# Optimization experiments

Measured on AMD Instinct MI355X. Metric: run time of the kernel, lower is better.

The kernel has to match this reference:

```python
import jax, jax.numpy as jnp
import numpy as np

K = 4  # Chebyshev order (layer._k)

def setup_inputs() -> dict:
    key = jax.random.key(0)
    k1, k2, k3, k4 = jax.random.split(key, 4)
    N, din, dout = 4096, 128, 128
    a = jax.random.normal(k1, (N, din), dtype=jnp.float32)            # layer input (only len used)
    r = jax.random.uniform(k2, (N, dout), dtype=jnp.float32)          # upstream relevance (positive)
    # sparse-ish binary directed adjacency, no self loops (avg degree ~16)
    adj = (jax.random.uniform(k3, (N, N)) < (16.0 / N)).astype(jnp.float32)
    adj = adj * (1.0 - jnp.eye(N, dtype=jnp.float32))
    W = jax.random.normal(k4, (dout, K * din), dtype=jnp.float32) * 0.05  # ChebConv linear weight [out, K*in]
    return {"a": a, "r": r, "adj": adj, "W": W}

def _forward(a, r, adj, W):
    N = a.shape[0]
    dW = W.shape[1] // K
    # Wk[k] = W[:, k*dW:(k+1)*dW].T  -> [K, dimY(in), dimJ(out)]; rho = abs
    rhoW = jnp.abs(jnp.stack([W[:, k * dW:(k + 1) * dW].T for k in range(K)]))
    # Laplacian: L = I - D^{-1/2} A D^{-1/2}, degrees clamped at 1 (in-degrees = column sums)
    dinv = jnp.clip(adj.sum(axis=0), 1.0, None) ** -0.5
    D = dinv[:, None] * adj * dinv[None, :]
    L = jnp.eye(N, dtype=adj.dtype) - D
    # Chebyshev polynomials T_0=I, T_1=L, T_k = 2 L T_{k-1} - T_{k-2}  -> [K, N, N]
    Ts = [jnp.eye(N, dtype=L.dtype), L]
    for _ in range(2, K):
        Ts.append(2.0 * (L @ Ts[-1]) - Ts[-2])
    Ak = jnp.stack(Ts[:K])
    # U[i,j,x,y] = sum_k Ak[k,i,x] * rhoW[k,y,j]; never materialized.
    # denom[i,j] = U.sum(dim=(2,3)) = sum_k (sum_x Ak[k,i,x]) * (sum_y rhoW[k,y,j])
    denom = jnp.einsum('ki,kj->ij', Ak.sum(axis=2), rhoW.sum(axis=1))
    c = r / denom
    # out[x,y] = einsum('ijxy,ij->xy', U, c) = sum_k Ak[k].T @ c @ rhoW[k].T
    return jnp.einsum('kix,kyj,ij->xy', Ak, rhoW, c)

def reference(a, r, adj, W):
    return _forward(a, r, adj, W)
```

## Files before the change

### kernel.cpp

```cpp
#include <hip/hip_runtime.h>
#include <cstdint>
#include <cstddef>

#define N_NODES 4096
#define FEAT 128
#define KCH 4
#define NNZ_CAP (1 << 18)
#define TB2 256
#define TB3 256
#define T2CAP 2048
#define RSTRIDE 96

__device__ __forceinline__ int panel_of(int p) {
    return p < 3456 ? (p / 384) : (p < 3776 ? 9 : 10);
}

__global__ __launch_bounds__(256) void k_adj(const float* __restrict__ adj,
                                             int* __restrict__ deg,
                                             int* __restrict__ rdeg,
                                             int* __restrict__ rcolF) {
    int row = (blockIdx.x * 256 + threadIdx.x) >> 6;
    int lane = threadIdx.x & 63;
    const float4* rowp = (const float4*)(adj + (size_t)row * N_NODES);
    int base = 0;
    for (int it = 0; it < 16; ++it) {
        float4 q = rowp[it * 64 + lane];
        int nib = (q.x != 0.0f) | ((q.y != 0.0f) << 1)
                | ((q.z != 0.0f) << 2) | ((q.w != 0.0f) << 3);
        int cnt = __popc(nib);
        int sc = cnt;
        for (int off = 1; off < 64; off <<= 1) {
            int n = __shfl_up(sc, off);
            if (lane >= off) sc += n;
        }
        int myoff = base + sc - cnt;
        int x0 = it * 256 + 4 * lane;
        #pragma unroll
        for (int c = 0; c < 4; ++c) {
            if (nib & (1 << c)) {
                if (myoff < RSTRIDE) rcolF[row * RSTRIDE + myoff] = x0 + c;
                atomicAdd(&deg[x0 + c], 1);
                ++myoff;
            }
        }
        base += __shfl(sc, 63);
    }
    if (lane == 0) rdeg[row] = (base > RSTRIDE) ? RSTRIDE : base;
}

__global__ __launch_bounds__(1024) void k_scan(const int* __restrict__ deg,
                                               float* __restrict__ dinv,
                                               int* __restrict__ colptr,
                                               int* __restrict__ colcur) {
    __shared__ int wsum[16];
    __shared__ int wbase[16];
    int t = threadIdx.x;
    int lane = t & 63, wv = t >> 6;
    int v[4]; int s = 0;
    for (int c = 0; c < 4; ++c) {
        int idx = t * 4 + c;
        int di = deg[idx];
        v[c] = di;
        s += di;
        float dc = fmaxf((float)di, 1.0f);
        dinv[idx] = (float)(1.0 / sqrt((double)dc));
    }
    int sc = s;
    for (int off = 1; off < 64; off <<= 1) {
        int n = __shfl_up(sc, off);
        if (lane >= off) sc += n;
    }
    if (lane == 63) wsum[wv] = sc;
    __syncthreads();
    if (t == 0) {
        int b = 0;
        for (int q2 = 0; q2 < 16; ++q2) { wbase[q2] = b; b += wsum[q2]; }
    }
    __syncthreads();
    int base = wbase[wv] + sc - s;
    for (int c = 0; c < 4; ++c) {
        int idx = t * 4 + c;
        colptr[idx] = base; colcur[idx] = base;
        base += v[c];
    }
    if (t == 1023) colptr[N_NODES] = base;
}

__global__ __launch_bounds__(256) void k_vals(const float* __restrict__ dinv,
                                              const int* __restrict__ rdeg,
                                              const int* __restrict__ rcolF,
                                              float* __restrict__ rlvalF,
                                              int* __restrict__ colcur,
                                              int* __restrict__ col_i,
                                              float* __restrict__ val,
                                              const float* __restrict__ W,
                                              float* __restrict__ sW) {
    if (blockIdx.x >= N_NODES / 4) {
        int tid = (blockIdx.x - N_NODES / 4) * 256 + threadIdx.x;
        int k = tid >> 7, j = tid & 127;
        float s = 0.f;
        for (int y = 0; y < FEAT; ++y)
            s += fabsf(W[(size_t)j * (KCH * FEAT) + k * FEAT + y]);
        sW[k * FEAT + j] = s;
        return;
    }
    int row = (blockIdx.x * 256 + threadIdx.x) >> 6;
    int lane = threadIdx.x & 63;
    int n = rdeg[row];
    float di = dinv[row];
    for (int e = lane; e < n; e += 64) {
        int x = rcolF[row * RSTRIDE + e];
        float dv = di * dinv[x];
        rlvalF[row * RSTRIDE + e] = -dv;
        int ec = atomicAdd(&colcur[x], 1);
        if (ec < NNZ_CAP) { col_i[ec] = row; val[ec] = dv; }
    }
}

__device__ __forceinline__ float np_pairwise_4096(const float* __restrict__ row,
                                                  float* r256, float* leaf,
                                                  float* bc, int t) {
    if (t < 256) {
        int L = t >> 3, j = t & 7;
        const float* p = row + L * 128 + j;
        float a = p[0];
        #pragma unroll
        for (int q = 1; q < 16; ++q) a += p[8 * q];
        r256[t] = a;
    }
    __syncthreads();
    if (t < 32) {
        const float* rr = r256 + t * 8;
        leaf[t] = ((rr[0] + rr[1]) + (rr[2] + rr[3])) + ((rr[4] + rr[5]) + (rr[6] + rr[7]));
    }
    __syncthreads();
    if (t == 0) {
        float v[32];
        #pragma unroll
        for (int q = 0; q < 32; ++q) v[q] = leaf[q];
        #pragma unroll
        for (int w = 16; w >= 1; w >>= 1)
            #pragma unroll
            for (int q = 0; q < 16; ++q)
                if (q < w) v[q] = v[2 * q] + v[2 * q + 1];
        bc[0] = v[0];
    }
    __syncthreads();
    float res = bc[0];
    __syncthreads();
    return res;
}

__global__ __launch_bounds__(TB2) void k_t2(const int* __restrict__ rdeg,
                                            const int* __restrict__ rcolF,
                                            const float* __restrict__ rlvalF,
                                            unsigned short* __restrict__ t2c,
                                            float* __restrict__ t2v,
                                            int* __restrict__ t2cnt,
                                            float* __restrict__ sA) {
    __shared__ float gp[N_NODES];
    __shared__ int   pcol[64];
    __shared__ float pLip[64];
    __shared__ int   pnn[64];
    __shared__ int   ssplit;
    __shared__ float r256[256], leaf[32], bc[1];
    __shared__ int   wtot[4], wbase[4];
    int t = threadIdx.x;
    int i = blockIdx.x;
    int rp = i * RSTRIDE;
    int ol = rdeg[i];
    int cnt = ol + 1;
    if (cnt > 64) cnt = 64;
    if (t == 0) ssplit = 0;
    __syncthreads();
    if (t < ol && rcolF[rp + t] < i) atomicAdd(&ssplit, 1);
    __syncthreads();
    int split = ssplit;
    if (t < cnt) {
        int col; float lip;
        if (t < split)       { col = rcolF[rp + t];     lip = rlvalF[rp + t]; }
        else if (t == split) { col = i;                 lip = 1.0f; }
        else                 { col = rcolF[rp + t - 1]; lip = rlvalF[rp + t - 1]; }
        pcol[t] = col; pLip[t] = lip; pnn[t] = rdeg[col];
    }
    float4* gp4 = (float4*)gp;
    const float4 z4 = make_float4(0.f, 0.f, 0.f, 0.f);
    #pragma unroll
    for (int u2 = 0; u2 < 4; ++u2) gp4[t + u2 * TB2] = z4;
    __syncthreads();
    for (int e = t; e < ol; e += TB2) gp[rcolF[rp + e]] = rlvalF[rp + e];
    if (t == 0) gp[i] = 1.0f;
    __syncthreads();
    float s1 = np_pairwise_4096(gp, r256, leaf, bc, t);
    for (int e = t; e < ol; e += TB2) gp[rcolF[rp + e]] = 0.0f;
    if (t == 0) gp[i] = 0.0f;
    __syncthreads();
    float tot[16];
    #pragma unroll
    for (int u = 0; u < 16; ++u) tot[u] = 0.0f;
    int q = 0;
    while (q < cnt) {
        {
            float lv = pLip[q];
            int p = pcol[q];
            int nn = pnn[q];
            int b = p * RSTRIDE;
            for (int e = t; e < nn; e += TB2)
                gp[rcolF[b + e]] = fmaf(lv, rlvalF[b + e], gp[rcolF[b + e]]);
            if (t == 0) gp[p] = fmaf(lv, 1.0f, gp[p]);
            __syncthreads();
        }
        ++q;
        if (q == cnt || panel_of(pcol[q]) != panel_of(pcol[q - 1])) {
            #pragma unroll
            for (int u2 = 0; u2 < 4; ++u2) {
                int idx = t + u2 * TB2;
                float4 b = gp4[idx];
                tot[4 * u2 + 0] = tot[4 * u2 + 0] + b.x;
                tot[4 * u2 + 1] = tot[4 * u2 + 1] + b.y;
                tot[4 * u2 + 2] = tot[4 * u2 + 2] + b.z;
                tot[4 * u2 + 3] = tot[4 * u2 + 3] + b.w;
                gp4[idx] = z4;
            }
            __syncthreads();
        }
    }
    #pragma unroll
    for (int u2 = 0; u2 < 4; ++u2) {
        int xb = 4 * t + 1024 * u2;
        float4 v;
        v.x = 2.0f * tot[4 * u2 + 0] - (xb + 0 == i ? 1.0f : 0.0f);
        v.y = 2.0f * tot[4 * u2 + 1] - (xb + 1 == i ? 1.0f : 0.0f);
        v.z = 2.0f * tot[4 * u2 + 2] - (xb + 2 == i ? 1.0f : 0.0f);
        v.w = 2.0f * tot[4 * u2 + 3] - (xb + 3 == i ? 1.0f : 0.0f);
        gp4[t + u2 * TB2] = v;
    }
    __syncthreads();
    float s2 = np_pairwise_4096(gp, r256, leaf, bc, t);
    float ev[16];
    #pragma unroll
    for (int u2 = 0; u2 < 4; ++u2) {
        float4 e4 = gp4[4 * t + u2];
        ev[4 * u2 + 0] = e4.x; ev[4 * u2 + 1] = e4.y;
        ev[4 * u2 + 2] = e4.z; ev[4 * u2 + 3] = e4.w;
    }
    int cl = 0;
    #pragma unroll
    for (int u = 0; u < 16; ++u) cl += (ev[u] != 0.0f);
    int lane = t & 63, wv = t >> 6;
    int sc = cl;
    for (int off = 1; off < 64; off <<= 1) {
        int n = __shfl_up(sc, off);
        if (lane >= off) sc += n;
    }
    if (lane == 63) wtot[wv] = sc;
    __syncthreads();
    if (t == 0) {
        int b = 0;
        for (int wq = 0; wq < 4; ++wq) { wbase[wq] = b; b += wtot[wq]; }
        t2cnt[i] = (b > T2CAP) ? T2CAP : b;
    }
    __syncthreads();
    int pos = wbase[wv] + sc - cl;
    unsigned short* dstc = t2c + (size_t)i * T2CAP;
    float* dstv = t2v + (size_t)i * T2CAP;
    #pragma unroll
    for (int u = 0; u < 16; ++u) {
        if (ev[u] != 0.0f) {
            if (pos < T2CAP) { dstc[pos] = (unsigned short)(t * 16 + u); dstv[pos] = ev[u]; }
            ++pos;
        }
    }
    if (t == 0) {
        sA[0 * N_NODES + i] = 1.0f;
        sA[1 * N_NODES + i] = s1;
        sA[2 * N_NODES + i] = s2;
    }
}

__global__ __launch_bounds__(TB3) void k_t3(const int* __restrict__ rdeg,
                                            const int* __restrict__ rcolF,
                                            const float* __restrict__ rlvalF,
                                            const unsigned short* __restrict__ t2c,
                                            const float* __restrict__ t2v,
                                            const int* __restrict__ t2cnt,
                                            float* __restrict__ sA) {
    __shared__ float gp[N_NODES];
    __shared__ int   pcol[64];
    __shared__ float pLip[64];
    __shared__ int   pnn[64];
    __shared__ int   ssplit;
    __shared__ float r256[256], leaf[32], bc[1];
    int t = threadIdx.x;
    int i = blockIdx.x;
    int rp = i * RSTRIDE;
    int ol = rdeg[i];
    int cnt = ol + 1;
    if (cnt > 64) cnt = 64;
    if (t == 0) ssplit = 0;
    __syncthreads();
    if (t < ol && rcolF[rp + t] < i) atomicAdd(&ssplit, 1);
    __syncthreads();
    int split = ssplit;
    if (t < cnt) {
        int col; float lip;
        if (t < split)       { col = rcolF[rp + t];     lip = rlvalF[rp + t]; }
        else if (t == split) { col = i;                  lip = 1.0f; }
        else                 { col = rcolF[rp + t - 1];  lip = rlvalF[rp + t - 1]; }
        pcol[t] = col; pLip[t] = lip; pnn[t] = t2cnt[col];
    }
    float4* gp4 = (float4*)gp;
    const float4 z4 = make_float4(0.f, 0.f, 0.f, 0.f);
    #pragma unroll
    for (int u2 = 0; u2 < 4; ++u2) gp4[t + u2 * TB3] = z4;
    __syncthreads();
    float tot[16];
    #pragma unroll
    for (int u = 0; u < 16; ++u) tot[u] = 0.0f;
    int q = 0;
    while (q < cnt) {
        {
            float lv = pLip[q];
            int nn = pnn[q];
            const unsigned short* spc = t2c + (size_t)pcol[q] * T2CAP;
            const float* spv = t2v + (size_t)pcol[q] * T2CAP;
            for (int e = t; e < nn; e += TB3) {
                int x = spc[e];
                gp[x] = fmaf(lv, spv[e], gp[x]);
            }
            __syncthreads();
        }
        ++q;
        if (q == cnt || panel_of(pcol[q]) != panel_of(pcol[q - 1])) {
            #pragma unroll
            for (int u2 = 0; u2 < 4; ++u2) {
                int idx = t + u2 * TB3;
                float4 b = gp4[idx];
                tot[4 * u2 + 0] = tot[4 * u2 + 0] + b.x;
                tot[4 * u2 + 1] = tot[4 * u2 + 1] + b.y;
                tot[4 * u2 + 2] = tot[4 * u2 + 2] + b.z;
                tot[4 * u2 + 3] = tot[4 * u2 + 3] + b.w;
                gp4[idx] = z4;
            }
            __syncthreads();
        }
    }
    #pragma unroll
    for (int u2 = 0; u2 < 4; ++u2) {
        float4 v;
        v.x = 2.0f * tot[4 * u2 + 0];
        v.y = 2.0f * tot[4 * u2 + 1];
        v.z = 2.0f * tot[4 * u2 + 2];
        v.w = 2.0f * tot[4 * u2 + 3];
        gp4[t + u2 * TB3] = v;
    }
    __syncthreads();
    for (int e = t; e < ol; e += TB3) { int x = rcolF[rp + e]; gp[x] = gp[x] - rlvalF[rp + e]; }
    if (t == 0) gp[i] = gp[i] - 1.0f;
    __syncthreads();
    float s3 = np_pairwise_4096(gp, r256, leaf, bc, t);
    if (t == 0) sA[3 * N_NODES + i] = s3;
}

__global__ __launch_bounds__(256) void k_cm(const float* __restrict__ r,
                                            const float* __restrict__ sA,
                                            const float* __restrict__ sW,
                                            const float* __restrict__ W,
                                            float* __restrict__ M) {
#pragma clang fp contract(off)
    __shared__ float cl[16][FEAT];
    int k = blockIdx.y;
    int ib = blockIdx.x * 16;
    int tx = threadIdx.x;
    int y = tx & 127, half = tx >> 7;
    for (int m = tx; m < 16 * FEAT; m += 256) {
        int i = ib + (m >> 7), j = m & 127;
        float denom = 0.0f;
        #pragma unroll
        for (int k2 = 0; k2 < KCH; ++k2) {
            float p = sA[k2 * N_NODES + i] * sW[k2 * FEAT + j];
            denom = denom + p;
        }
        cl[m >> 7][m & 127] = r[(size_t)i * FEAT + j] / denom;
    }
    __syncthreads();
    float acc[8];
    #pragma unroll
    for (int u = 0; u < 8; ++u) acc[u] = 0.0f;
    for (int j = 0; j < FEAT; ++j) {
        float a = fabsf(W[(size_t)j * (KCH * FEAT) + k * FEAT + y]);
        #pragma unroll
        for (int u = 0; u < 8; ++u) acc[u] += a * cl[half * 8 + u][j];
    }
    #pragma unroll
    for (int u = 0; u < 8; ++u)
        M[(size_t)k * N_NODES * FEAT + (size_t)(ib + half * 8 + u) * FEAT + y] = acc[u];
}

__global__ void k_h1(const int* __restrict__ colptr, const int* __restrict__ col_i,
                     const float* __restrict__ val, const float* __restrict__ M,
                     float* __restrict__ B2) {
    int x = blockIdx.x * 2 + (threadIdx.x >> 7);
    int y = threadIdx.x & 127;
    const float* M2 = M + (size_t)2 * N_NODES * FEAT;
    const float* M3 = M + (size_t)3 * N_NODES * FEAT;
    int e0 = colptr[x], e1 = colptr[x + 1];
    if (e1 > NNZ_CAP) e1 = NNZ_CAP;
    float g = 0.0f;
    for (int e = e0; e < e1; ++e)
        g += val[e] * M3[(size_t)col_i[e] * FEAT + y];
    size_t o = (size_t)x * FEAT + y;
    B2[o] = 2.0f * M2[o] + 4.0f * (M3[o] - g);
}

__global__ void k_h2(const int* __restrict__ colptr, const int* __restrict__ col_i,
                     const float* __restrict__ val, const float* __restrict__ M,
                     const float* __restrict__ B2, float* __restrict__ B3) {
    int x = blockIdx.x * 2 + (threadIdx.x >> 7);
    int y = threadIdx.x & 127;
    const float* M1 = M + (size_t)N_NODES * FEAT;
    const float* M3 = M + (size_t)3 * N_NODES * FEAT;
    int e0 = colptr[x], e1 = colptr[x + 1];
    if (e1 > NNZ_CAP) e1 = NNZ_CAP;
    float g = 0.0f;
    for (int e = e0; e < e1; ++e)
        g += val[e] * B2[(size_t)col_i[e] * FEAT + y];
    size_t o = (size_t)x * FEAT + y;
    B3[o] = (M1[o] - 3.0f * M3[o]) + (B2[o] - g);
}

__global__ void k_h3(const int* __restrict__ colptr, const int* __restrict__ col_i,
                     const float* __restrict__ val, const float* __restrict__ M,
                     const float* __restrict__ B3, float* __restrict__ out) {
    int x = blockIdx.x * 2 + (threadIdx.x >> 7);
    int y = threadIdx.x & 127;
    const float* M0 = M;
    const float* M2 = M + (size_t)2 * N_NODES * FEAT;
    int e0 = colptr[x], e1 = colptr[x + 1];
    if (e1 > NNZ_CAP) e1 = NNZ_CAP;
    float g = 0.0f;
    for (int e = e0; e < e1; ++e)
        g += val[e] * B3[(size_t)col_i[e] * FEAT + y];
    size_t o = (size_t)x * FEAT + y;
    out[o] = (M0[o] - M2[o]) + (B3[o] - g);
}

extern "C" void kernel_launch(void* const* d_in, const int* in_sizes, int n_in,
                              void* d_out, int out_size, void* d_ws, size_t ws_size,
                              hipStream_t stream) {
    const float* r   = (const float*)d_in[1];
    const float* adj = (const float*)d_in[2];
    const float* W   = (const float*)d_in[3];
    float* out = (float*)d_out;

    char* w = (char*)d_ws;
    auto take = [&](size_t bytes) {
        char* p = w;
        w += (bytes + 255) & ~(size_t)255;
        return p;
    };
    int*   deg    = (int*)take((size_t)N_NODES * 4);
    int*   rdeg   = (int*)take((size_t)N_NODES * 4);
    float* dinv   = (float*)take((size_t)N_NODES * 4);
    int*   colcur = (int*)take((size_t)N_NODES * 4);
    int*   colptr = (int*)take((size_t)(N_NODES + 1) * 4);
    int*   col_i  = (int*)take((size_t)NNZ_CAP * 4);
    float* val    = (float*)take((size_t)NNZ_CAP * 4);
    int*   rcolF  = (int*)take((size_t)N_NODES * RSTRIDE * 4);
    float* rlvalF = (float*)take((size_t)N_NODES * RSTRIDE * 4);
    float* sW     = (float*)take((size_t)KCH * FEAT * 4);
    float* sA     = (float*)take((size_t)KCH * N_NODES * 4);
    float* M      = (float*)take((size_t)KCH * N_NODES * FEAT * 4);
    float* B2     = (float*)take((size_t)N_NODES * FEAT * 4);
    float* B3     = (float*)take((size_t)N_NODES * FEAT * 4);
    int*   t2cnt  = (int*)take((size_t)N_NODES * 4);
    unsigned short* t2c = (unsigned short*)take((size_t)N_NODES * T2CAP * 2);
    float* t2v    = (float*)take((size_t)N_NODES * T2CAP * 4);

    hipMemsetAsync(deg, 0, (size_t)N_NODES * 4, stream);
    k_adj<<<N_NODES / 4, 256, 0, stream>>>(adj, deg, rdeg, rcolF);
    k_scan<<<1, 1024, 0, stream>>>(deg, dinv, colptr, colcur);
    k_vals<<<N_NODES / 4 + 2, 256, 0, stream>>>(dinv, rdeg, rcolF, rlvalF,
                                                colcur, col_i, val, W, sW);
    k_t2<<<N_NODES, TB2, 0, stream>>>(rdeg, rcolF, rlvalF, t2c, t2v, t2cnt, sA);
    k_t3<<<N_NODES, TB3, 0, stream>>>(rdeg, rcolF, rlvalF, t2c, t2v, t2cnt, sA);
    k_cm<<<dim3(N_NODES / 16, KCH), 256, 0, stream>>>(r, sA, sW, W, M);
    k_h1<<<N_NODES / 2, 256, 0, stream>>>(colptr, col_i, val, M, B2);
    k_h2<<<N_NODES / 2, 256, 0, stream>>>(colptr, col_i, val, M, B2, B3);
    k_h3<<<N_NODES / 2, 256, 0, stream>>>(colptr, col_i, val, M, B3, out);
}
```

Measured before the change: 306.6 us.

## Split T2/T3 row expansion into two column-half blocks with separate leaf reduction

```diff
diff --git a/kernel.cpp b/kernel.cpp
--- a/kernel.cpp
+++ b/kernel.cpp
@@ -6,9 +6,9 @@
 #define FEAT 128
 #define KCH 4
 #define NNZ_CAP (1 << 18)
-#define TB2 256
-#define TB3 256
-#define T2CAP 2048
+#define TBH 128
+#define HALF 2048
+#define T2HC 1024
 #define RSTRIDE 96
 
 __device__ __forceinline__ int panel_of(int p) {
@@ -117,56 +117,40 @@
     }
 }
 
-__device__ __forceinline__ float np_pairwise_4096(const float* __restrict__ row,
-                                                  float* r256, float* leaf,
-                                                  float* bc, int t) {
-    if (t < 256) {
-        int L = t >> 3, j = t & 7;
-        const float* p = row + L * 128 + j;
-        float a = p[0];
-        #pragma unroll
-        for (int q = 1; q < 16; ++q) a += p[8 * q];
-        r256[t] = a;
-    }
-    __syncthreads();
-    if (t < 32) {
-        const float* rr = r256 + t * 8;
-        leaf[t] = ((rr[0] + rr[1]) + (rr[2] + rr[3])) + ((rr[4] + rr[5]) + (rr[6] + rr[7]));
-    }
-    __syncthreads();
-    if (t == 0) {
-        float v[32];
-        #pragma unroll
-        for (int q = 0; q < 32; ++q) v[q] = leaf[q];
-        #pragma unroll
-        for (int w = 16; w >= 1; w >>= 1)
-            #pragma unroll
-            for (int q = 0; q < 16; ++q)
-                if (q < w) v[q] = v[2 * q] + v[2 * q + 1];
-        bc[0] = v[0];
-    }
-    __syncthreads();
-    float res = bc[0];
-    __syncthreads();
-    return res;
-}
-
-__global__ __launch_bounds__(TB2) void k_t2(const int* __restrict__ rdeg,
+__device__ __forceinline__ void np_leaves_half(const float* __restrict__ half,
+                                               float* r256h, float* lf, int t) {
+    const float* p = half + (t >> 3) * 128 + (t & 7);
+    float a = p[0];
+    #pragma unroll
+    for (int q = 1; q < 16; ++q) a += p[8 * q];
+    r256h[t] = a;
+    __syncthreads();
+    if (t < 16) {
+        const float* rr = r256h + t * 8;
+        lf[t] = ((rr[0] + rr[1]) + (rr[2] + rr[3])) + ((rr[4] + rr[5]) + (rr[6] + rr[7]));
+    }
+    __syncthreads();
+}
+
+__global__ __launch_bounds__(TBH) void k_t2(const int* __restrict__ rdeg,
                                             const int* __restrict__ rcolF,
                                             const float* __restrict__ rlvalF,
                                             unsigned short* __restrict__ t2c,
                                             float* __restrict__ t2v,
-                                            int* __restrict__ t2cnt,
-                                            float* __restrict__ sA) {
-    __shared__ float gp[N_NODES];
+                                            int* __restrict__ t2cnt2,
+                                            float* __restrict__ L1f,
+                                            float* __restrict__ L2f) {
+    __shared__ float gp[HALF];
     __shared__ int   pcol[64];
     __shared__ float pLip[64];
     __shared__ int   pnn[64];
     __shared__ int   ssplit;
-    __shared__ float r256[256], leaf[32], bc[1];
-    __shared__ int   wtot[4], wbase[4];
+    __shared__ float r256h[TBH], lf[16];
+    __shared__ int   wtot[2], wbase2[2];
     int t = threadIdx.x;
-    int i = blockIdx.x;
+    int bid = blockIdx.x;
+    int i = bid >> 1, h = bid & 1;
+    int base = h << 11;
     int rp = i * RSTRIDE;
     int ol = rdeg[i];
     int cnt = ol + 1;
@@ -186,14 +170,22 @@
     float4* gp4 = (float4*)gp;
     const float4 z4 = make_float4(0.f, 0.f, 0.f, 0.f);
     #pragma unroll
-    for (int u2 = 0; u2 < 4; ++u2) gp4[t + u2 * TB2] = z4;
-    __syncthreads();
-    for (int e = t; e < ol; e += TB2) gp[rcolF[rp + e]] = rlvalF[rp + e];
-    if (t == 0) gp[i] = 1.0f;
-    __syncthreads();
-    float s1 = np_pairwise_4096(gp, r256, leaf, bc, t);
-    for (int e = t; e < ol; e += TB2) gp[rcolF[rp + e]] = 0.0f;
-    if (t == 0) gp[i] = 0.0f;
+    for (int u2 = 0; u2 < 4; ++u2) gp4[t + u2 * TBH] = z4;
+    __syncthreads();
+    for (int e = t; e < ol; e += TBH) {
+        int x = rcolF[rp + e];
+        if ((x >> 11) == h) gp[x - base] = rlvalF[rp + e];
+    }
+    if (t == 0 && (i >> 11) == h) gp[i - base] = 1.0f;
+    __syncthreads();
+    np_leaves_half(gp, r256h, lf, t);
+    if (t < 16) L1f[(size_t)i * 32 + h * 16 + t] = lf[t];
+    __syncthreads();
+    for (int e = t; e < ol; e += TBH) {
+        int x = rcolF[rp + e];
+        if ((x >> 11) == h) gp[x - base] = 0.0f;
+    }
+    if (t == 0 && (i >> 11) == h) gp[i - base] = 0.0f;
     __syncthreads();
     float tot[16];
     #pragma unroll
@@ -205,21 +197,23 @@
             int p = pcol[q];
             int nn = pnn[q];
             int b = p * RSTRIDE;
-            for (int e = t; e < nn; e += TB2)
-                gp[rcolF[b + e]] = fmaf(lv, rlvalF[b + e], gp[rcolF[b + e]]);
-            if (t == 0) gp[p] = fmaf(lv, 1.0f, gp[p]);
+            for (int e = t; e < nn; e += TBH) {
+                int x = rcolF[b + e];
+                if ((x >> 11) == h) gp[x - base] = fmaf(lv, rlvalF[b + e], gp[x - base]);
+            }
+            if (t == 0 && (p >> 11) == h) gp[p - base] = fmaf(lv, 1.0f, gp[p - base]);
             __syncthreads();
         }
         ++q;
         if (q == cnt || panel_of(pcol[q]) != panel_of(pcol[q - 1])) {
             #pragma unroll
             for (int u2 = 0; u2 < 4; ++u2) {
-                int idx = t + u2 * TB2;
-                float4 b = gp4[idx];
-                tot[4 * u2 + 0] = tot[4 * u2 + 0] + b.x;
-                tot[4 * u2 + 1] = tot[4 * u2 + 1] + b.y;
-                tot[4 * u2 + 2] = tot[4 * u2 + 2] + b.z;
-                tot[4 * u2 + 3] = tot[4 * u2 + 3] + b.w;
+                int idx = t + u2 * TBH;
+                float4 b4 = gp4[idx];
+                tot[4 * u2 + 0] = tot[4 * u2 + 0] + b4.x;
+                tot[4 * u2 + 1] = tot[4 * u2 + 1] + b4.y;
+                tot[4 * u2 + 2] = tot[4 * u2 + 2] + b4.z;
+                tot[4 * u2 + 3] = tot[4 * u2 + 3] + b4.w;
                 gp4[idx] = z4;
             }
             __syncthreads();
@@ -227,16 +221,17 @@
     }
     #pragma unroll
     for (int u2 = 0; u2 < 4; ++u2) {
-        int xb = 4 * t + 1024 * u2;
+        int xg = base + 4 * t + 512 * u2;
         float4 v;
-        v.x = 2.0f * tot[4 * u2 + 0] - (xb + 0 == i ? 1.0f : 0.0f);
-        v.y = 2.0f * tot[4 * u2 + 1] - (xb + 1 == i ? 1.0f : 0.0f);
-        v.z = 2.0f * tot[4 * u2 + 2] - (xb + 2 == i ? 1.0f : 0.0f);
-        v.w = 2.0f * tot[4 * u2 + 3] - (xb + 3 == i ? 1.0f : 0.0f);
-        gp4[t + u2 * TB2] = v;
-    }
-    __syncthreads();
-    float s2 = np_pairwise_4096(gp, r256, leaf, bc, t);
+        v.x = 2.0f * tot[4 * u2 + 0] - (xg + 0 == i ? 1.0f : 0.0f);
+        v.y = 2.0f * tot[4 * u2 + 1] - (xg + 1 == i ? 1.0f : 0.0f);
+        v.z = 2.0f * tot[4 * u2 + 2] - (xg + 2 == i ? 1.0f : 0.0f);
+        v.w = 2.0f * tot[4 * u2 + 3] - (xg + 3 == i ? 1.0f : 0.0f);
+        gp4[t + u2 * TBH] = v;
+    }
+    __syncthreads();
+    np_leaves_half(gp, r256h, lf, t);
+    if (t < 16) L2f[(size_t)i * 32 + h * 16 + t] = lf[t];
     float ev[16];
     #pragma unroll
     for (int u2 = 0; u2 < 4; ++u2) {
@@ -256,43 +251,44 @@
     if (lane == 63) wtot[wv] = sc;
     __syncthreads();
     if (t == 0) {
-        int b = 0;
-        for (int wq = 0; wq < 4; ++wq) { wbase[wq] = b; b += wtot[wq]; }
-        t2cnt[i] = (b > T2CAP) ? T2CAP : b;
-    }
-    __syncthreads();
-    int pos = wbase[wv] + sc - cl;
-    unsigned short* dstc = t2c + (size_t)i * T2CAP;
-    float* dstv = t2v + (size_t)i * T2CAP;
+        int b = wtot[0];
+        wbase2[0] = 0; wbase2[1] = b;
+        b += wtot[1];
+        t2cnt2[bid] = (b > T2HC) ? T2HC : b;
+    }
+    __syncthreads();
+    int pos = wbase2[wv] + sc - cl;
+    unsigned short* dstc = t2c + (size_t)bid * T2HC;
+    float* dstv = t2v + (size_t)bid * T2HC;
     #pragma unroll
     for (int u = 0; u < 16; ++u) {
         if (ev[u] != 0.0f) {
-            if (pos < T2CAP) { dstc[pos] = (unsigned short)(t * 16 + u); dstv[pos] = ev[u]; }
+            if (pos < T2HC) {
+                dstc[pos] = (unsigned short)(base + t * 16 + u);
+                dstv[pos] = ev[u];
+            }
             ++pos;
         }
     }
-    if (t == 0) {
-        sA[0 * N_NODES + i] = 1.0f;
-        sA[1 * N_NODES + i] = s1;
-        sA[2 * N_NODES + i] = s2;
-    }
-}
-
-__global__ __launch_bounds__(TB3) void k_t3(const int* __restrict__ rdeg,
+}
+
+__global__ __launch_bounds__(TBH) void k_t3(const int* __restrict__ rdeg,
                                             const int* __restrict__ rcolF,
                                             const float* __restrict__ rlvalF,
                                             const unsigned short* __restrict__ t2c,
                                             const float* __restrict__ t2v,
-                                            const int* __restrict__ t2cnt,
-                                            float* __restrict__ sA) {
-    __shared__ float gp[N_NODES];
+                                            const int* __restrict__ t2cnt2,
+                                            float* __restrict__ L3f) {
+    __shared__ float gp[HALF];
     __shared__ int   pcol[64];
     __shared__ float pLip[64];
     __shared__ int   pnn[64];
     __shared__ int   ssplit;
-    __shared__ float r256[256], leaf[32], bc[1];
+    __shared__ float r256h[TBH], lf[16];
     int t = threadIdx.x;
-    int i = blockIdx.x;
+    int bid = blockIdx.x;
+    int i = bid >> 1, h = bid & 1;
+    int base = h << 11;
     int rp = i * RSTRIDE;
     int ol = rdeg[i];
     int cnt = ol + 1;
@@ -307,12 +303,12 @@
         if (t < split)       { col = rcolF[rp + t];     lip = rlvalF[rp + t]; }
         else if (t == split) { col = i;                  lip = 1.0f; }
         else                 { col = rcolF[rp + t - 1];  lip = rlvalF[rp + t - 1]; }
-        pcol[t] = col; pLip[t] = lip; pnn[t] = t2cnt[col];
+        pcol[t] = col; pLip[t] = lip; pnn[t] = t2cnt2[col * 2 + h];
     }
     float4* gp4 = (float4*)gp;
     const float4 z4 = make_float4(0.f, 0.f, 0.f, 0.f);
     #pragma unroll
-    for (int u2 = 0; u2 < 4; ++u2) gp4[t + u2 * TB3] = z4;
+    for (int u2 = 0; u2 < 4; ++u2) gp4[t + u2 * TBH] = z4;
     __syncthreads();
     float tot[16];
     #pragma unroll
@@ -322,11 +318,12 @@
         {
             float lv = pLip[q];
             int nn = pnn[q];
-            const unsigned short* spc = t2c + (size_t)pcol[q] * T2CAP;
-            const float* spv = t2v + (size_t)pcol[q] * T2CAP;
-            for (int e = t; e < nn; e += TB3) {
+            size_t seg = (size_t)(pcol[q] * 2 + h) * T2HC;
+            const unsigned short* spc = t2c + seg;
+            const float* spv = t2v + seg;
+            for (int e = t; e < nn; e += TBH) {
                 int x = spc[e];
-                gp[x] = fmaf(lv, spv[e], gp[x]);
+                gp[x - base] = fmaf(lv, spv[e], gp[x - base]);
             }
             __syncthreads();
         }
@@ -334,12 +331,12 @@
         if (q == cnt || panel_of(pcol[q]) != panel_of(pcol[q - 1])) {
             #pragma unroll
             for (int u2 = 0; u2 < 4; ++u2) {
-                int idx = t + u2 * TB3;
-                float4 b = gp4[idx];
-                tot[4 * u2 + 0] = tot[4 * u2 + 0] + b.x;
-                tot[4 * u2 + 1] = tot[4 * u2 + 1] + b.y;
-                tot[4 * u2 + 2] = tot[4 * u2 + 2] + b.z;
-                tot[4 * u2 + 3] = tot[4 * u2 + 3] + b.w;
+                int idx = t + u2 * TBH;
+                float4 b4 = gp4[idx];
+                tot[4 * u2 + 0] = tot[4 * u2 + 0] + b4.x;
+                tot[4 * u2 + 1] = tot[4 * u2 + 1] + b4.y;
+                tot[4 * u2 + 2] = tot[4 * u2 + 2] + b4.z;
+                tot[4 * u2 + 3] = tot[4 * u2 + 3] + b4.w;
                 gp4[idx] = z4;
             }
             __syncthreads();
@@ -352,14 +349,39 @@
         v.y = 2.0f * tot[4 * u2 + 1];
         v.z = 2.0f * tot[4 * u2 + 2];
         v.w = 2.0f * tot[4 * u2 + 3];
-        gp4[t + u2 * TB3] = v;
-    }
-    __syncthreads();
-    for (int e = t; e < ol; e += TB3) { int x = rcolF[rp + e]; gp[x] = gp[x] - rlvalF[rp + e]; }
-    if (t == 0) gp[i] = gp[i] - 1.0f;
-    __syncthreads();
-    float s3 = np_pairwise_4096(gp, r256, leaf, bc, t);
-    if (t == 0) sA[3 * N_NODES + i] = s3;
+        gp4[t + u2 * TBH] = v;
+    }
+    __syncthreads();
+    for (int e = t; e < ol; e += TBH) {
+        int x = rcolF[rp + e];
+        if ((x >> 11) == h) gp[x - base] = gp[x - base] - rlvalF[rp + e];
+    }
+    if (t == 0 && (i >> 11) == h) gp[i - base] = gp[i - base] - 1.0f;
+    __syncthreads();
+    np_leaves_half(gp, r256h, lf, t);
+    if (t < 16) L3f[(size_t)i * 32 + h * 16 + t] = lf[t];
+}
+
+__global__ __launch_bounds__(256) void k_s(const float* __restrict__ L1f,
+                                           const float* __restrict__ L2f,
+                                           const float* __restrict__ L3f,
+                                           float* __restrict__ sA) {
+    int i = blockIdx.x * 256 + threadIdx.x;
+    const float* srcs[3] = {L1f + (size_t)i * 32, L2f + (size_t)i * 32, L3f + (size_t)i * 32};
+    #pragma unroll
+    for (int s = 0; s < 3; ++s) {
+        const float* Lp = srcs[s];
+        float v[32];
+        #pragma unroll
+        for (int q = 0; q < 32; ++q) v[q] = Lp[q];
+        #pragma unroll
+        for (int w = 16; w >= 1; w >>= 1)
+            #pragma unroll
+            for (int q = 0; q < 16; ++q)
+                if (q < w) v[q] = v[2 * q] + v[2 * q + 1];
+        sA[(s + 1) * N_NODES + i] = v[0];
+    }
+    sA[i] = 1.0f;
 }
 
 __global__ __launch_bounds__(256) void k_cm(const float* __restrict__ r,
@@ -473,17 +495,22 @@
     float* M      = (float*)take((size_t)KCH * N_NODES * FEAT * 4);
     float* B2     = (float*)take((size_t)N_NODES * FEAT * 4);
     float* B3     = (float*)take((size_t)N_NODES * FEAT * 4);
-    int*   t2cnt  = (int*)take((size_t)N_NODES * 4);
-    unsigned short* t2c = (unsigned short*)take((size_t)N_NODES * T2CAP * 2);
-    float* t2v    = (float*)take((size_t)N_NODES * T2CAP * 4);
+    int*   t2cnt2 = (int*)take((size_t)N_NODES * 2 * 4);
+    unsigned short* t2c = (unsigned short*)take((size_t)N_NODES * 2 * T2HC * 2);
+    float* t2v    = (float*)take((size_t)N_NODES * 2 * T2HC * 4);
+    float* L1f    = (float*)take((size_t)N_NODES * 32 * 4);
+    float* L2f    = (float*)take((size_t)N_NODES * 32 * 4);
+    float* L3f    = (float*)take((size_t)N_NODES * 32 * 4);
 
     hipMemsetAsync(deg, 0, (size_t)N_NODES * 4, stream);
     k_adj<<<N_NODES / 4, 256, 0, stream>>>(adj, deg, rdeg, rcolF);
     k_scan<<<1, 1024, 0, stream>>>(deg, dinv, colptr, colcur);
     k_vals<<<N_NODES / 4 + 2, 256, 0, stream>>>(dinv, rdeg, rcolF, rlvalF,
                                                 colcur, col_i, val, W, sW);
-    k_t2<<<N_NODES, TB2, 0, stream>>>(rdeg, rcolF, rlvalF, t2c, t2v, t2cnt, sA);
-    k_t3<<<N_NODES, TB3, 0, stream>>>(rdeg, rcolF, rlvalF, t2c, t2v, t2cnt, sA);
+    k_t2<<<N_NODES * 2, TBH, 0, stream>>>(rdeg, rcolF, rlvalF, t2c, t2v, t2cnt2,
+                                          L1f, L2f);
+    k_t3<<<N_NODES * 2, TBH, 0, stream>>>(rdeg, rcolF, rlvalF, t2c, t2v, t2cnt2, L3f);
+    k_s<<<N_NODES / 256, 256, 0, stream>>>(L1f, L2f, L3f, sA);
     k_cm<<<dim3(N_NODES / 16, KCH), 256, 0, stream>>>(r, sA, sW, W, M);
     k_h1<<<N_NODES / 2, 256, 0, stream>>>(colptr, col_i, val, M, B2);
     k_h2<<<N_NODES / 2, 256, 0, stream>>>(colptr, col_i, val, M, B2, B3);
```

New measurement: 311.0 us. No clear change (+1.4%).

## Process two rows per k_t3 block with 512 threads and shared barriers

Applied to the files above, without the earlier changes.

```diff
diff --git a/kernel.cpp b/kernel.cpp
--- a/kernel.cpp
+++ b/kernel.cpp
@@ -7,7 +7,7 @@
 #define KCH 4
 #define NNZ_CAP (1 << 18)
 #define TB2 256
-#define TB3 256
+#define TB3 512
 #define T2CAP 2048
 #define RSTRIDE 96
 
@@ -285,81 +285,131 @@
                                             const float* __restrict__ t2v,
                                             const int* __restrict__ t2cnt,
                                             float* __restrict__ sA) {
-    __shared__ float gp[N_NODES];
-    __shared__ int   pcol[64];
-    __shared__ float pLip[64];
-    __shared__ int   pnn[64];
-    __shared__ int   ssplit;
+    __shared__ float gp0[N_NODES];
+    __shared__ float gp1[N_NODES];
+    __shared__ int   pcol0[64], pcol1[64];
+    __shared__ float pLip0[64], pLip1[64];
+    __shared__ int   pnn0[64], pnn1[64];
+    __shared__ int   ssplit0, ssplit1;
     __shared__ float r256[256], leaf[32], bc[1];
     int t = threadIdx.x;
-    int i = blockIdx.x;
-    int rp = i * RSTRIDE;
-    int ol = rdeg[i];
-    int cnt = ol + 1;
-    if (cnt > 64) cnt = 64;
-    if (t == 0) ssplit = 0;
-    __syncthreads();
-    if (t < ol && rcolF[rp + t] < i) atomicAdd(&ssplit, 1);
-    __syncthreads();
-    int split = ssplit;
-    if (t < cnt) {
+    int i0 = blockIdx.x * 2, i1 = i0 + 1;
+    int rp0 = i0 * RSTRIDE, rp1 = i1 * RSTRIDE;
+    int ol0 = rdeg[i0], ol1 = rdeg[i1];
+    int cnt0 = ol0 + 1; if (cnt0 > 64) cnt0 = 64;
+    int cnt1 = ol1 + 1; if (cnt1 > 64) cnt1 = 64;
+    if (t == 0) { ssplit0 = 0; ssplit1 = 0; }
+    __syncthreads();
+    if (t < ol0 && rcolF[rp0 + t] < i0) atomicAdd(&ssplit0, 1);
+    if (t < ol1 && rcolF[rp1 + t] < i1) atomicAdd(&ssplit1, 1);
+    __syncthreads();
+    int split0 = ssplit0, split1 = ssplit1;
+    if (t < cnt0) {
         int col; float lip;
-        if (t < split)       { col = rcolF[rp + t];     lip = rlvalF[rp + t]; }
-        else if (t == split) { col = i;                  lip = 1.0f; }
-        else                 { col = rcolF[rp + t - 1];  lip = rlvalF[rp + t - 1]; }
-        pcol[t] = col; pLip[t] = lip; pnn[t] = t2cnt[col];
-    }
-    float4* gp4 = (float4*)gp;
+        if (t < split0)       { col = rcolF[rp0 + t];     lip = rlvalF[rp0 + t]; }
+        else if (t == split0) { col = i0;                  lip = 1.0f; }
+        else                  { col = rcolF[rp0 + t - 1];  lip = rlvalF[rp0 + t - 1]; }
+        pcol0[t] = col; pLip0[t] = lip; pnn0[t] = t2cnt[col];
+    }
+    if (t < cnt1) {
+        int col; float lip;
+        if (t < split1)       { col = rcolF[rp1 + t];     lip = rlvalF[rp1 + t]; }
+        else if (t == split1) { col = i1;                  lip = 1.0f; }
+        else                  { col = rcolF[rp1 + t - 1];  lip = rlvalF[rp1 + t - 1]; }
+        pcol1[t] = col; pLip1[t] = lip; pnn1[t] = t2cnt[col];
+    }
+    float4* g04 = (float4*)gp0;
+    float4* g14 = (float4*)gp1;
     const float4 z4 = make_float4(0.f, 0.f, 0.f, 0.f);
     #pragma unroll
-    for (int u2 = 0; u2 < 4; ++u2) gp4[t + u2 * TB3] = z4;
-    __syncthreads();
-    float tot[16];
-    #pragma unroll
-    for (int u = 0; u < 16; ++u) tot[u] = 0.0f;
+    for (int u2 = 0; u2 < 2; ++u2) { g04[t + u2 * TB3] = z4; g14[t + u2 * TB3] = z4; }
+    __syncthreads();
+    float tot0[8], tot1[8];
+    #pragma unroll
+    for (int u = 0; u < 8; ++u) { tot0[u] = 0.0f; tot1[u] = 0.0f; }
+    int mx = (cnt0 > cnt1) ? cnt0 : cnt1;
     int q = 0;
-    while (q < cnt) {
-        {
-            float lv = pLip[q];
-            int nn = pnn[q];
-            const unsigned short* spc = t2c + (size_t)pcol[q] * T2CAP;
-            const float* spv = t2v + (size_t)pcol[q] * T2CAP;
+    while (q < mx) {
+        if (q < cnt0) {
+            float lv = pLip0[q];
+            int nn = pnn0[q];
+            size_t seg = (size_t)pcol0[q] * T2CAP;
+            const unsigned short* spc = t2c + seg;
+            const float* spv = t2v + seg;
             for (int e = t; e < nn; e += TB3) {
                 int x = spc[e];
-                gp[x] = fmaf(lv, spv[e], gp[x]);
+                gp0[x] = fmaf(lv, spv[e], gp0[x]);
             }
-            __syncthreads();
-        }
+        }
+        if (q < cnt1) {
+            float lv = pLip1[q];
+            int nn = pnn1[q];
+            size_t seg = (size_t)pcol1[q] * T2CAP;
+            const unsigned short* spc = t2c + seg;
+            const float* spv = t2v + seg;
+            for (int e = t; e < nn; e += TB3) {
+                int x = spc[e];
+                gp1[x] = fmaf(lv, spv[e], gp1[x]);
+            }
+        }
+        __syncthreads();
+        bool f0 = (q < cnt0) && (q + 1 == cnt0 || panel_of(pcol0[q + 1]) != panel_of(pcol0[q]));
+        bool f1 = (q < cnt1) && (q + 1 == cnt1 || panel_of(pcol1[q + 1]) != panel_of(pcol1[q]));
+        if (f0) {
+            #pragma unroll
+            for (int u2 = 0; u2 < 2; ++u2) {
+                int idx = t + u2 * TB3;
+                float4 b4 = g04[idx];
+                tot0[4 * u2 + 0] = tot0[4 * u2 + 0] + b4.x;
+                tot0[4 * u2 + 1] = tot0[4 * u2 + 1] + b4.y;
+                tot0[4 * u2 + 2] = tot0[4 * u2 + 2] + b4.z;
+                tot0[4 * u2 + 3] = tot0[4 * u2 + 3] + b4.w;
+                g04[idx] = z4;
+            }
+        }
+        if (f1) {
+            #pragma unroll
+            for (int u2 = 0; u2 < 2; ++u2) {
+                int idx = t + u2 * TB3;
+                float4 b4 = g14[idx];
+                tot1[4 * u2 + 0] = tot1[4 * u2 + 0] + b4.x;
+                tot1[4 * u2 + 1] = tot1[4 * u2 + 1] + b4.y;
+                tot1[4 * u2 + 2] = tot1[4 * u2 + 2] + b4.z;
+                tot1[4 * u2 + 3] = tot1[4 * u2 + 3] + b4.w;
+                g14[idx] = z4;
+            }
+        }
+        if (f0 || f1) __syncthreads();
         ++q;
-        if (q == cnt || panel_of(pcol[q]) != panel_of(pcol[q - 1])) {
-            #pragma unroll
-            for (int u2 = 0; u2 < 4; ++u2) {
-                int idx = t + u2 * TB3;
-                float4 b = gp4[idx];
-                tot[4 * u2 + 0] = tot[4 * u2 + 0] + b.x;
-                tot[4 * u2 + 1] = tot[4 * u2 + 1] + b.y;
-                tot[4 * u2 + 2] = tot[4 * u2 + 2] + b.z;
-                tot[4 * u2 + 3] = tot[4 * u2 + 3] + b.w;
-                gp4[idx] = z4;
-            }
-            __syncthreads();
-        }
-    }
-    #pragma unroll
-    for (int u2 = 0; u2 < 4; ++u2) {
-        float4 v;
-        v.x = 2.0f * tot[4 * u2 + 0];
-        v.y = 2.0f * tot[4 * u2 + 1];
-        v.z = 2.0f * tot[4 * u2 + 2];
-        v.w = 2.0f * tot[4 * u2 + 3];
-        gp4[t + u2 * TB3] = v;
-    }
-    __syncthreads();
-    for (int e = t; e < ol; e += TB3) { int x = rcolF[rp + e]; gp[x] = gp[x] - rlvalF[rp + e]; }
-    if (t == 0) gp[i] = gp[i] - 1.0f;
-    __syncthreads();
-    float s3 = np_pairwise_4096(gp, r256, leaf, bc, t);
-    if (t == 0) sA[3 * N_NODES + i] = s3;
+    }
+    #pragma unroll
+    for (int u2 = 0; u2 < 2; ++u2) {
+        float4 v0, v1;
+        v0.x = 2.0f * tot0[4 * u2 + 0]; v0.y = 2.0f * tot0[4 * u2 + 1];
+        v0.z = 2.0f * tot0[4 * u2 + 2]; v0.w = 2.0f * tot0[4 * u2 + 3];
+        v1.x = 2.0f * tot1[4 * u2 + 0]; v1.y = 2.0f * tot1[4 * u2 + 1];
+        v1.z = 2.0f * tot1[4 * u2 + 2]; v1.w = 2.0f * tot1[4 * u2 + 3];
+        g04[t + u2 * TB3] = v0;
+        g14[t + u2 * TB3] = v1;
+    }
+    __syncthreads();
+    for (int e = t; e < ol0; e += TB3) {
+        int x = rcolF[rp0 + e];
+        gp0[x] = gp0[x] - rlvalF[rp0 + e];
+    }
+    if (t == 0) gp0[i0] = gp0[i0] - 1.0f;
+    for (int e = t; e < ol1; e += TB3) {
+        int x = rcolF[rp1 + e];
+        gp1[x] = gp1[x] - rlvalF[rp1 + e];
+    }
+    if (t == 0) gp1[i1] = gp1[i1] - 1.0f;
+    __syncthreads();
+    float s3a = np_pairwise_4096(gp0, r256, leaf, bc, t);
+    float s3b = np_pairwise_4096(gp1, r256, leaf, bc, t);
+    if (t == 0) {
+        sA[3 * N_NODES + i0] = s3a;
+        sA[3 * N_NODES + i1] = s3b;
+    }
 }
 
 __global__ __launch_bounds__(256) void k_cm(const float* __restrict__ r,
@@ -483,7 +533,7 @@
     k_vals<<<N_NODES / 4 + 2, 256, 0, stream>>>(dinv, rdeg, rcolF, rlvalF,
                                                 colcur, col_i, val, W, sW);
     k_t2<<<N_NODES, TB2, 0, stream>>>(rdeg, rcolF, rlvalF, t2c, t2v, t2cnt, sA);
-    k_t3<<<N_NODES, TB3, 0, stream>>>(rdeg, rcolF, rlvalF, t2c, t2v, t2cnt, sA);
+    k_t3<<<N_NODES / 2, TB3, 0, stream>>>(rdeg, rcolF, rlvalF, t2c, t2v, t2cnt, sA);
     k_cm<<<dim3(N_NODES / 16, KCH), 256, 0, stream>>>(r, sA, sW, W, M);
     k_h1<<<N_NODES / 2, 256, 0, stream>>>(colptr, col_i, val, M, B2);
     k_h2<<<N_NODES / 2, 256, 0, stream>>>(colptr, col_i, val, M, B2, B3);
```

After: 329.3 us. 1.07x slower.
